# Performance work log

Measured on AMD Instinct MI355X. Metric: run time of the kernel, lower is better.

The kernel has to match this reference:

```python
import jax, jax.numpy as jnp
import numpy as np

NUM_GROUPS = 50000
NUM_ITEMS = 100000
NUM_NODES = NUM_GROUPS + NUM_ITEMS
NUM_EDGES = 2400000
EMBED_DIM = 64
LAYERS = 3


def setup_inputs() -> dict:
    key = jax.random.key(0)
    k1, k2, k3, k4, k5 = jax.random.split(key, 5)
    groups_emb = jax.random.normal(k1, (NUM_GROUPS, EMBED_DIM), dtype=jnp.float32)
    items_emb = jax.random.normal(k2, (NUM_ITEMS, EMBED_DIM), dtype=jnp.float32)
    # COO representation of the symmetric-normalized adjacency (values ~ 1/deg)
    edge_rows = jax.random.randint(k3, (NUM_EDGES,), 0, NUM_NODES, dtype=jnp.int32)
    edge_cols = jax.random.randint(k4, (NUM_EDGES,), 0, NUM_NODES, dtype=jnp.int32)
    edge_vals = jax.random.uniform(k5, (NUM_EDGES,), dtype=jnp.float32) * 0.1
    return {
        "groups_emb": groups_emb,
        "items_emb": items_emb,
        "edge_vals": edge_vals,
        "edge_rows": edge_rows,
        "edge_cols": edge_cols,
    }


def _spmm(edge_rows, edge_cols, edge_vals, x):
    # y[r] = sum_{e: rows[e]==r} vals[e] * x[cols[e]]   == torch.sparse.mm(A, x)
    msgs = edge_vals[:, None] * x[edge_cols]  # [E, d] gather + scale
    return jax.ops.segment_sum(msgs, edge_rows, num_segments=NUM_NODES)


def reference(groups_emb, items_emb, edge_vals, edge_rows, edge_cols):
    all_emb = jnp.concatenate([groups_emb, items_emb], axis=0)  # [N, d]
    acc = all_emb  # running sum of layer embeddings (fused mean)
    x = all_emb
    for _ in range(LAYERS):
        x = _spmm(edge_rows, edge_cols, edge_vals, x)
        acc = acc + x
    mean_emb = acc / jnp.asarray(LAYERS + 1, dtype=acc.dtype)
    groups = mean_emb[:NUM_GROUPS]
    return groups
```

## Files before the change

kernel.cpp:

```cpp
#include <hip/hip_runtime.h>

#define NGROUPS 50000
#define NITEMS  100000
#define NNODES  150000
#define NEDGES  2400000
#define DIM     64
#define BROWS   128
#define NBKT    ((NNODES + BROWS - 1) / BROWS)
#define NPB     256

__device__ __forceinline__ ushort f2bf(float f) {
    unsigned u = __float_as_uint(f);
    u += 0x7FFF + ((u >> 16) & 1);
    return (ushort)(u >> 16);
}
__device__ __forceinline__ float bf2f(ushort h) {
    return __uint_as_float((unsigned)h << 16);
}
__device__ __forceinline__ float bflo(int u) { return __uint_as_float((unsigned)u << 16); }
__device__ __forceinline__ float bfhi(int u) { return __uint_as_float((unsigned)u & 0xFFFF0000u); }
__device__ __forceinline__ int pack2(float lo, float hi) {
    return (int)f2bf(lo) | ((int)f2bf(hi) << 16);
}


__global__ __launch_bounds__(256) void k_tobf16(const float4* __restrict__ g,
                                                const float4* __restrict__ it,
                                                ushort4* __restrict__ xb) {
    const int n1 = NGROUPS * DIM / 4;
    const int n  = NNODES * DIM / 4;
    int i = blockIdx.x * blockDim.x + threadIdx.x;
    int s = gridDim.x * blockDim.x;
    for (; i < n; i += s) {
        float4 v = (i < n1) ? g[i] : it[i - n1];
        ushort4 h;
        h.x = f2bf(v.x); h.y = f2bf(v.y); h.z = f2bf(v.z); h.w = f2bf(v.w);
        xb[i] = h;
    }
}

__global__ __launch_bounds__(512) void k_bcount(const int4* __restrict__ rows4,
                                                int* __restrict__ bh) {
    __shared__ int h[NBKT];
    for (int i = threadIdx.x; i < NBKT; i += 512) h[i] = 0;
    __syncthreads();
    const int per4 = (NEDGES / 4 + NPB - 1) / NPB;
    int b4 = blockIdx.x * per4;
    int e4 = min(b4 + per4, NEDGES / 4);
    for (int i = b4 + threadIdx.x; i < e4; i += 512) {
        int4 r = rows4[i];
        atomicAdd(&h[r.x >> 7], 1);
        atomicAdd(&h[r.y >> 7], 1);
        atomicAdd(&h[r.z >> 7], 1);
        atomicAdd(&h[r.w >> 7], 1);
    }
    __syncthreads();
    for (int i = threadIdx.x; i < NBKT; i += 512)
        bh[(size_t)i * NPB + blockIdx.x] = h[i];
}

__global__ __launch_bounds__(256) void k_bktscan(int* __restrict__ bh,
                                                 int* __restrict__ btot) {
    __shared__ int s[NPB];
    int b = blockIdx.x, t = threadIdx.x;
    int v = bh[(size_t)b * NPB + t];
    s[t] = v;
    __syncthreads();
    for (int off = 1; off < NPB; off <<= 1) {
        int u = (t >= off) ? s[t - off] : 0;
        __syncthreads();
        s[t] += u;
        __syncthreads();
    }
    bh[(size_t)b * NPB + t] = s[t] - v;
    if (t == NPB - 1) btot[b] = s[t];
}

__global__ __launch_bounds__(1024) void k_bbase(const int* __restrict__ btot,
                                                int* __restrict__ bbase) {
    __shared__ int s[2048];
    int t = threadIdx.x;
    int v1 = (t < NBKT) ? btot[t] : 0;
    int v2 = (t + 1024 < NBKT) ? btot[t + 1024] : 0;
    s[t] = v1; s[t + 1024] = v2;
    __syncthreads();
    for (int off = 1; off < 2048; off <<= 1) {
        int u1 = (t >= off) ? s[t - off] : 0;
        int u2 = s[t + 1024 - off];
        __syncthreads();
        s[t] += u1; s[t + 1024] += u2;
        __syncthreads();
    }
    if (t < NBKT) bbase[t] = s[t] - v1;
    if (t + 1024 < NBKT) bbase[t + 1024] = s[t + 1024] - v2;
    if (t == 0) bbase[NBKT] = NEDGES;
}

__global__ __launch_bounds__(512) void k_bin(const int4* __restrict__ rows4,
                                             const int4* __restrict__ cols4,
                                             const float4* __restrict__ vals4,
                                             const int* __restrict__ bh,
                                             const int* __restrict__ bbase,
                                             int2* __restrict__ evt) {
    __shared__ int cur[NBKT];
    for (int i = threadIdx.x; i < NBKT; i += 512)
        cur[i] = bbase[i] + bh[(size_t)i * NPB + blockIdx.x];
    __syncthreads();
    const int per4 = (NEDGES / 4 + NPB - 1) / NPB;
    int b4 = blockIdx.x * per4;
    int e4 = min(b4 + per4, NEDGES / 4);
    for (int i = b4 + threadIdx.x; i < e4; i += 512) {
        int4   r = rows4[i];
        int4   c = cols4[i];
        float4 v = vals4[i];
        int p0 = atomicAdd(&cur[r.x >> 7], 1);
        int p1 = atomicAdd(&cur[r.y >> 7], 1);
        int p2 = atomicAdd(&cur[r.z >> 7], 1);
        int p3 = atomicAdd(&cur[r.w >> 7], 1);
        evt[p0] = make_int2(c.x | ((r.x & 127) << 18), __float_as_int(v.x));
        evt[p1] = make_int2(c.y | ((r.y & 127) << 18), __float_as_int(v.y));
        evt[p2] = make_int2(c.z | ((r.z & 127) << 18), __float_as_int(v.z));
        evt[p3] = make_int2(c.w | ((r.w & 127) << 18), __float_as_int(v.w));
    }
}

__global__ __launch_bounds__(256) void k_sort2(const int2* __restrict__ evt,
                                               const int* __restrict__ bbase,
                                               int2* __restrict__ scv,
                                               int* __restrict__ rowptr) {
    __shared__ int h[BROWS];
    __shared__ int curp[BROWS];
    int b = blockIdx.x, t = threadIdx.x;
    int beg = bbase[b], end = bbase[b + 1];
    int rbase = b * BROWS;

    if (t < BROWS) h[t] = 0;
    __syncthreads();
    for (int j = beg + t; j < end; j += 256)
        atomicAdd(&h[evt[j].x >> 18], 1);
    __syncthreads();
    int cnt = (t < BROWS) ? h[t] : 0;
    for (int off = 1; off < BROWS; off <<= 1) {
        int u = (t < BROWS && t >= off) ? h[t - off] : 0;
        __syncthreads();
        if (t < BROWS) h[t] += u;
        __syncthreads();
    }
    if (t < BROWS) {
        int excl = beg + h[t] - cnt;
        curp[t] = excl;
        int r = rbase + t;
        if (r < NNODES) rowptr[r] = excl;
        if (r == NNODES - 1) rowptr[NNODES] = NEDGES;
    }
    __syncthreads();
    for (int j = beg + t; j < end; j += 256) {
        int2 e = evt[j];
        int  p = atomicAdd(&curp[e.x >> 18], 1);
        scv[p] = make_int2(e.x & 0x3FFFF, e.y);
    }
}

template <int LAYER>
__global__ __launch_bounds__(256) void k_spmm_csr(const int* __restrict__ rowptr,
                                                  const int2* __restrict__ scv,
                                                  const ushort* __restrict__ xsrc,
                                                  const float4* __restrict__ groups4,
                                                  ushort* __restrict__ y,
                                                  float4* __restrict__ out4) {
    int r    = blockIdx.x * 4 + (threadIdx.x >> 6);
    int lane = threadIdx.x & 63;
    int q    = lane >> 3;
    int sl   = lane & 7;
    int beg = rowptr[r], end = rowptr[r + 1];

    float a0 = 0.f, a1 = 0.f, a2 = 0.f, a3 = 0.f;
    float a4 = 0.f, a5 = 0.f, a6 = 0.f, a7 = 0.f;

    int j = beg + q;
    for (; j + 8 < end; j += 16) {
        int2  cv0 = scv[j];
        int2  cv1 = scv[j + 8];
        float v0  = __int_as_float(cv0.y);
        float v1  = __int_as_float(cv1.y);
        int4 h0 = ((const int4*)(xsrc + (size_t)cv0.x * DIM))[sl];
        int4 h1 = ((const int4*)(xsrc + (size_t)cv1.x * DIM))[sl];
        a0 = fmaf(v0, bflo(h0.x), a0); a1 = fmaf(v0, bfhi(h0.x), a1);
        a2 = fmaf(v0, bflo(h0.y), a2); a3 = fmaf(v0, bfhi(h0.y), a3);
        a4 = fmaf(v0, bflo(h0.z), a4); a5 = fmaf(v0, bfhi(h0.z), a5);
        a6 = fmaf(v0, bflo(h0.w), a6); a7 = fmaf(v0, bfhi(h0.w), a7);
        a0 = fmaf(v1, bflo(h1.x), a0); a1 = fmaf(v1, bfhi(h1.x), a1);
        a2 = fmaf(v1, bflo(h1.y), a2); a3 = fmaf(v1, bfhi(h1.y), a3);
        a4 = fmaf(v1, bflo(h1.z), a4); a5 = fmaf(v1, bfhi(h1.z), a5);
        a6 = fmaf(v1, bflo(h1.w), a6); a7 = fmaf(v1, bfhi(h1.w), a7);
    }
    if (j < end) {
        int2  cv = scv[j];
        float v  = __int_as_float(cv.y);
        int4 h = ((const int4*)(xsrc + (size_t)cv.x * DIM))[sl];
        a0 = fmaf(v, bflo(h.x), a0); a1 = fmaf(v, bfhi(h.x), a1);
        a2 = fmaf(v, bflo(h.y), a2); a3 = fmaf(v, bfhi(h.y), a3);
        a4 = fmaf(v, bflo(h.z), a4); a5 = fmaf(v, bfhi(h.z), a5);
        a6 = fmaf(v, bflo(h.w), a6); a7 = fmaf(v, bfhi(h.w), a7);
    }

    #define RED1(a) a += __shfl_xor(a, 8, 64); a += __shfl_xor(a, 16, 64); a += __shfl_xor(a, 32, 64);
    RED1(a0) RED1(a1) RED1(a2) RED1(a3) RED1(a4) RED1(a5) RED1(a6) RED1(a7)
    #undef RED1

    if (lane < 16) {
        int half = lane >> 3;
        float b0 = half ? a4 : a0, b1 = half ? a5 : a1;
        float b2 = half ? a6 : a2, b3 = half ? a7 : a3;
        if (LAYER != 3) {
            int2 w;
            w.x = pack2(b0, b1);
            w.y = pack2(b2, b3);
            ((int2*)(y + (size_t)r * DIM))[sl * 2 + half] = w;
        }
        size_t o = (size_t)r * 16 + sl * 2 + half;
        if (LAYER == 1) {
            if (r < NGROUPS) out4[o] = make_float4(b0, b1, b2, b3);
        } else if (LAYER == 2) {
            if (r < NGROUPS) {
                float4 a = out4[o];
                a.x += b0; a.y += b1; a.z += b2; a.w += b3;
                out4[o] = a;
            }
        } else {
            float4 a = out4[o];
            float4 g = groups4[o];
            a.x = (a.x + g.x + b0) * 0.25f;
            a.y = (a.y + g.y + b1) * 0.25f;
            a.z = (a.z + g.z + b2) * 0.25f;
            a.w = (a.w + g.w + b3) * 0.25f;
            out4[o] = a;
        }
    }
}


__global__ __launch_bounds__(256) void k_zero(float4* __restrict__ p, int n4) {
    int i = blockIdx.x * blockDim.x + threadIdx.x;
    int s = gridDim.x * blockDim.x;
    float4 z = make_float4(0.f, 0.f, 0.f, 0.f);
    for (; i < n4; i += s) p[i] = z;
}

__global__ __launch_bounds__(256) void k_concat(const float4* __restrict__ g,
                                                const float4* __restrict__ it,
                                                float4* __restrict__ x) {
    const int n1 = NGROUPS * DIM / 4;
    const int n  = NNODES * DIM / 4;
    int i = blockIdx.x * blockDim.x + threadIdx.x;
    int s = gridDim.x * blockDim.x;
    for (; i < n; i += s) x[i] = (i < n1) ? g[i] : it[i - n1];
}

__global__ __launch_bounds__(256) void k_spmm(const int*   __restrict__ rows,
                                              const int*   __restrict__ cols,
                                              const float* __restrict__ vals,
                                              const float* __restrict__ x,
                                              float*       __restrict__ y) {
    int wid  = (blockIdx.x * blockDim.x + threadIdx.x) >> 6;
    int lane = threadIdx.x & 63;
    int nw   = (gridDim.x * blockDim.x) >> 6;
    for (int e = wid; e < NEDGES; e += nw) {
        int   r = rows[e];
        int   c = cols[e];
        float v = vals[e];
        unsafeAtomicAdd(&y[r * DIM + lane], v * x[c * DIM + lane]);
    }
}

__global__ __launch_bounds__(256) void k_accum(const float4* __restrict__ src,
                                               float4* __restrict__ dst, int first) {
    const int n = NGROUPS * DIM / 4;
    int i = blockIdx.x * blockDim.x + threadIdx.x;
    int s = gridDim.x * blockDim.x;
    if (first) { for (; i < n; i += s) dst[i] = src[i]; }
    else {
        for (; i < n; i += s) {
            float4 a = dst[i], b = src[i];
            a.x += b.x; a.y += b.y; a.z += b.z; a.w += b.w;
            dst[i] = a;
        }
    }
}

__global__ __launch_bounds__(256) void k_final(const float4* __restrict__ g,
                                               float4* __restrict__ out) {
    const int n = NGROUPS * DIM / 4;
    int i = blockIdx.x * blockDim.x + threadIdx.x;
    int s = gridDim.x * blockDim.x;
    for (; i < n; i += s) {
        float4 a = out[i], b = g[i];
        out[i] = make_float4((a.x + b.x) * 0.25f, (a.y + b.y) * 0.25f,
                             (a.z + b.z) * 0.25f, (a.w + b.w) * 0.25f);
    }
}


extern "C" void kernel_launch(void* const* d_in, const int* in_sizes, int n_in,
                              void* d_out, int out_size, void* d_ws, size_t ws_size,
                              hipStream_t stream) {
    const float* groups = (const float*)d_in[0];
    const float* items  = (const float*)d_in[1];
    const float* vals   = (const float*)d_in[2];
    const int*   rows   = (const int*)d_in[3];
    const int*   cols   = (const int*)d_in[4];
    float* out = (float*)d_out;

    size_t off = 0;
    float* x1     = (float*)d_ws;                off += (size_t)NNODES * DIM;
    float* x2     = (float*)d_ws + off;          off += (size_t)NNODES * DIM;
    int2*  scv    = (int2*)((float*)d_ws + off); off += (size_t)NEDGES * 2;
    float* x0     = (float*)d_ws + off;          off += (size_t)NNODES * DIM / 2;
    int*   rowptr = (int*)((float*)d_ws + off);  off += NNODES + 4;
    int*   bbase  = (int*)((float*)d_ws + off);  off += 1280;
    int*   btot   = (int*)((float*)d_ws + off);  off += 1280;
    size_t needed = off * sizeof(float);

    ushort* x0b = (ushort*)x0;
    ushort* x1b = (ushort*)x1;
    ushort* x2b = (ushort*)x2;
    int*  bh  = (int*)x1;
    int2* evt = (int2*)x2;

    dim3 blk(256);

    if (ws_size >= needed) {
        k_tobf16<<<1024, blk, 0, stream>>>((const float4*)groups, (const float4*)items,
                                           (ushort4*)x0b);
        k_bcount<<<NPB, dim3(512), 0, stream>>>((const int4*)rows, bh);
        k_bktscan<<<NBKT, dim3(NPB), 0, stream>>>(bh, btot);
        k_bbase<<<1, dim3(1024), 0, stream>>>(btot, bbase);
        k_bin<<<NPB, dim3(512), 0, stream>>>((const int4*)rows, (const int4*)cols,
                                             (const float4*)vals, bh, bbase, evt);
        k_sort2<<<NBKT, blk, 0, stream>>>(evt, bbase, scv, rowptr);

        k_spmm_csr<1><<<NNODES / 4, blk, 0, stream>>>(rowptr, scv, x0b,
                                                      (const float4*)groups, x1b,
                                                      (float4*)out);
        k_spmm_csr<2><<<NNODES / 4, blk, 0, stream>>>(rowptr, scv, x1b,
                                                      (const float4*)groups, x2b,
                                                      (float4*)out);
        k_spmm_csr<3><<<NGROUPS / 4, blk, 0, stream>>>(rowptr, scv, x2b,
                                                       (const float4*)groups, nullptr,
                                                       (float4*)out);
    } else {
        float* xA = x1;
        float* xB = x2;
        k_concat<<<2048, blk, 0, stream>>>((const float4*)groups, (const float4*)items,
                                           (float4*)xA);
        for (int l = 0; l < 3; ++l) {
            k_zero<<<2048, blk, 0, stream>>>((float4*)xB, NNODES * DIM / 4);
            k_spmm<<<4096, blk, 0, stream>>>(rows, cols, vals, xA, xB);
            k_accum<<<512, blk, 0, stream>>>((const float4*)xB, (float4*)out, l == 0);
            float* t = xA; xA = xB; xB = t;
        }
        k_final<<<512, blk, 0, stream>>>((const float4*)groups, (float4*)out);
    }
}
```

Before: 315.7 us.

## Map one 8-lane slice per row in CSR SpMM instead of one wavefront

Each 64-lane wavefront now handles 8 rows, with each 8-lane slice owning one row and walking its edges sequentially, where before the whole wavefront shared one row and split its edges across slices. This drops the cross-slice shuffle reduction and lets every lane write its own 8 outputs directly. With about 16 edges per row, the old mapping left many slices idle on short rows. The trade-off is longer serial edge loops per slice and divergence when row lengths within a wavefront differ.

```diff
diff --git a/kernel.cpp b/kernel.cpp
--- a/kernel.cpp
+++ b/kernel.cpp
@@ -168,19 +168,23 @@
                                                   const float4* __restrict__ groups4,
                                                   ushort* __restrict__ y,
                                                   float4* __restrict__ out4) {
-    int r    = blockIdx.x * 4 + (threadIdx.x >> 6);
-    int lane = threadIdx.x & 63;
-    int q    = lane >> 3;
-    int sl   = lane & 7;
+    int wid   = threadIdx.x >> 6;
+    int lane  = threadIdx.x & 63;
+    int slice = lane >> 3;
+    int sl    = lane & 7;
+
+    int r = blockIdx.x * 32 + wid * 8 + slice;
+    const int RLIM = (LAYER == 3) ? NGROUPS : NNODES;
+    if (r >= RLIM) return;
     int beg = rowptr[r], end = rowptr[r + 1];
 
     float a0 = 0.f, a1 = 0.f, a2 = 0.f, a3 = 0.f;
     float a4 = 0.f, a5 = 0.f, a6 = 0.f, a7 = 0.f;
 
-    int j = beg + q;
-    for (; j + 8 < end; j += 16) {
+    int j = beg;
+    for (; j + 1 < end; j += 2) {
         int2  cv0 = scv[j];
-        int2  cv1 = scv[j + 8];
+        int2  cv1 = scv[j + 1];
         float v0  = __int_as_float(cv0.y);
         float v1  = __int_as_float(cv1.y);
         int4 h0 = ((const int4*)(xsrc + (size_t)cv0.x * DIM))[sl];
@@ -204,38 +208,37 @@
         a6 = fmaf(v, bflo(h.w), a6); a7 = fmaf(v, bfhi(h.w), a7);
     }
 
-    #define RED1(a) a += __shfl_xor(a, 8, 64); a += __shfl_xor(a, 16, 64); a += __shfl_xor(a, 32, 64);
-    RED1(a0) RED1(a1) RED1(a2) RED1(a3) RED1(a4) RED1(a5) RED1(a6) RED1(a7)
-    #undef RED1
-
-    if (lane < 16) {
-        int half = lane >> 3;
-        float b0 = half ? a4 : a0, b1 = half ? a5 : a1;
-        float b2 = half ? a6 : a2, b3 = half ? a7 : a3;
-        if (LAYER != 3) {
-            int2 w;
-            w.x = pack2(b0, b1);
-            w.y = pack2(b2, b3);
-            ((int2*)(y + (size_t)r * DIM))[sl * 2 + half] = w;
+    if (LAYER != 3) {
+        int4 w;
+        w.x = pack2(a0, a1); w.y = pack2(a2, a3);
+        w.z = pack2(a4, a5); w.w = pack2(a6, a7);
+        ((int4*)(y + (size_t)r * DIM))[sl] = w;
+    }
+    size_t o = (size_t)r * 16 + sl * 2;
+    if (LAYER == 1) {
+        if (r < NGROUPS) {
+            out4[o]     = make_float4(a0, a1, a2, a3);
+            out4[o + 1] = make_float4(a4, a5, a6, a7);
         }
-        size_t o = (size_t)r * 16 + sl * 2 + half;
-        if (LAYER == 1) {
-            if (r < NGROUPS) out4[o] = make_float4(b0, b1, b2, b3);
-        } else if (LAYER == 2) {
-            if (r < NGROUPS) {
-                float4 a = out4[o];
-                a.x += b0; a.y += b1; a.z += b2; a.w += b3;
-                out4[o] = a;
-            }
-        } else {
-            float4 a = out4[o];
-            float4 g = groups4[o];
-            a.x = (a.x + g.x + b0) * 0.25f;
-            a.y = (a.y + g.y + b1) * 0.25f;
-            a.z = (a.z + g.z + b2) * 0.25f;
-            a.w = (a.w + g.w + b3) * 0.25f;
-            out4[o] = a;
+    } else if (LAYER == 2) {
+        if (r < NGROUPS) {
+            float4 p = out4[o], q = out4[o + 1];
+            p.x += a0; p.y += a1; p.z += a2; p.w += a3;
+            q.x += a4; q.y += a5; q.z += a6; q.w += a7;
+            out4[o] = p; out4[o + 1] = q;
         }
+    } else {
+        float4 p = out4[o], q = out4[o + 1];
+        float4 gp = groups4[o], gq = groups4[o + 1];
+        p.x = (p.x + gp.x + a0) * 0.25f;
+        p.y = (p.y + gp.y + a1) * 0.25f;
+        p.z = (p.z + gp.z + a2) * 0.25f;
+        p.w = (p.w + gp.w + a3) * 0.25f;
+        q.x = (q.x + gq.x + a4) * 0.25f;
+        q.y = (q.y + gq.y + a5) * 0.25f;
+        q.z = (q.z + gq.z + a6) * 0.25f;
+        q.w = (q.w + gq.w + a7) * 0.25f;
+        out4[o] = p; out4[o + 1] = q;
     }
 }
 
@@ -339,15 +342,17 @@
                                              (const float4*)vals, bh, bbase, evt);
         k_sort2<<<NBKT, blk, 0, stream>>>(evt, bbase, scv, rowptr);
 
-        k_spmm_csr<1><<<NNODES / 4, blk, 0, stream>>>(rowptr, scv, x0b,
-                                                      (const float4*)groups, x1b,
-                                                      (float4*)out);
-        k_spmm_csr<2><<<NNODES / 4, blk, 0, stream>>>(rowptr, scv, x1b,
-                                                      (const float4*)groups, x2b,
-                                                      (float4*)out);
-        k_spmm_csr<3><<<NGROUPS / 4, blk, 0, stream>>>(rowptr, scv, x2b,
-                                                       (const float4*)groups, nullptr,
-                                                       (float4*)out);
+        const int GB1 = (NNODES + 31) / 32;
+        const int GB3 = (NGROUPS + 31) / 32;
+        k_spmm_csr<1><<<GB1, blk, 0, stream>>>(rowptr, scv, x0b,
+                                               (const float4*)groups, x1b,
+                                               (float4*)out);
+        k_spmm_csr<2><<<GB1, blk, 0, stream>>>(rowptr, scv, x1b,
+                                               (const float4*)groups, x2b,
+                                               (float4*)out);
+        k_spmm_csr<3><<<GB3, blk, 0, stream>>>(rowptr, scv, x2b,
+                                               (const float4*)groups, nullptr,
+                                               (float4*)out);
     } else {
         float* xA = x1;
         float* xB = x2;
```

Result: faster. 303.1 us (-4.0%).
